# Optimization experiments

Hardware: AMD Instinct MI355X
Metric: run time of the kernel (lower is better)

The kernel has to match this reference:

```python
import jax, jax.numpy as jnp
import numpy as np

WIDTH = 1024

def setup_inputs() -> dict:
    key = jax.random.key(0)
    ks = jax.random.split(key, 5)
    x = jax.random.normal(ks[0], (4, 4096, WIDTH), dtype=jnp.float32)
    # LayerNorm params
    ln_gamma = jnp.ones((WIDTH,), dtype=jnp.float32)
    ln_beta = jnp.zeros((WIDTH,), dtype=jnp.float32)
    # Linear params (torch nn.Linear init: U(-1/sqrt(fan_in), 1/sqrt(fan_in)))
    bound = 1.0 / np.sqrt(WIDTH)
    w1 = jax.random.uniform(ks[1], (WIDTH, WIDTH), jnp.float32, -bound, bound)
    b1 = jax.random.uniform(ks[2], (WIDTH,), jnp.float32, -bound, bound)
    w2 = jax.random.uniform(ks[3], (WIDTH, WIDTH), jnp.float32, -bound, bound)
    b2 = jax.random.uniform(ks[4], (WIDTH,), jnp.float32, -bound, bound)
    return {"x": x, "ln_gamma": ln_gamma, "ln_beta": ln_beta,
            "w1": w1, "b1": b1, "w2": w2, "b2": b2}

def _layernorm(x, gamma, beta, eps=1e-5):
    mu = jnp.mean(x, axis=-1, keepdims=True)
    var = jnp.mean(jnp.square(x - mu), axis=-1, keepdims=True)
    return (x - mu) * jax.lax.rsqrt(var + eps) * gamma + beta

def reference(x, ln_gamma, ln_beta, w1, b1, w2, b2):
    # Pre-norm residual MLP: x + W2 @ gelu(W1 @ LN(x) + b1) + b2
    h = _layernorm(x, ln_gamma, ln_beta)
    h = jnp.einsum('bsd,ed->bse', h, w1) + b1  # w stored as [out, in] like torch
    h = jax.nn.gelu(h, approximate=False)      # torch nn.GELU default = exact erf
    # dropout p=0.0 -> identity
    h = jnp.einsum('bsd,ed->bse', h, w2) + b2
    return x + h
```

## Files before the change

kernel.cpp:

```cpp
#include <hip/hip_runtime.h>
#include <hip/hip_bf16.h>
#include <math.h>

typedef __bf16 bf16x8 __attribute__((ext_vector_type(8)));
typedef float f32x4 __attribute__((ext_vector_type(4)));

#define GAS __attribute__((address_space(1)))
#define LAS __attribute__((address_space(3)))

static __device__ __forceinline__ void load16(const void* g, void* l) {
    __builtin_amdgcn_global_load_lds((const GAS void*)g, (LAS void*)l, 16, 0, 0);
}

struct __align__(8) bh4 { __hip_bfloat16 x, y, z, w; };

__global__ __launch_bounds__(256) void pre_kernel(
        const float* __restrict__ x, const float* __restrict__ gamma,
        const float* __restrict__ beta, const float* __restrict__ w1,
        const float* __restrict__ w2, __hip_bfloat16* __restrict__ hn,
        __hip_bfloat16* __restrict__ w1b, __hip_bfloat16* __restrict__ w2b, int nln) {
    if ((int)blockIdx.x >= nln) {
        const int i = (blockIdx.x - nln) * 256 + threadIdx.x;
        float4 a = ((const float4*)w1)[i];
        float4 b = ((const float4*)w2)[i];
        bh4 r1, r2;
        r1.x = __float2bfloat16(a.x); r1.y = __float2bfloat16(a.y);
        r1.z = __float2bfloat16(a.z); r1.w = __float2bfloat16(a.w);
        r2.x = __float2bfloat16(b.x); r2.y = __float2bfloat16(b.y);
        r2.z = __float2bfloat16(b.z); r2.w = __float2bfloat16(b.w);
        ((bh4*)w1b)[i] = r1;
        ((bh4*)w2b)[i] = r2;
        return;
    }
    const int row  = (blockIdx.x << 2) + (threadIdx.x >> 6);
    const int lane = threadIdx.x & 63;
    const float4* px = (const float4*)(x + (size_t)row * 1024);
    float4 v[4];
    float s = 0.f;
#pragma unroll
    for (int i = 0; i < 4; ++i) {
        v[i] = px[lane + (i << 6)];
        s += v[i].x + v[i].y + v[i].z + v[i].w;
    }
#pragma unroll
    for (int o = 32; o; o >>= 1) s += __shfl_xor(s, o, 64);
    const float mu = s * (1.0f / 1024.0f);
    float vs = 0.f;
#pragma unroll
    for (int i = 0; i < 4; ++i) {
        float a = v[i].x - mu, b = v[i].y - mu, c = v[i].z - mu, d = v[i].w - mu;
        vs += a * a + b * b + c * c + d * d;
    }
#pragma unroll
    for (int o = 32; o; o >>= 1) vs += __shfl_xor(vs, o, 64);
    const float rs = rsqrtf(vs * (1.0f / 1024.0f) + 1e-5f);
    const float4* pg = (const float4*)gamma;
    const float4* pb = (const float4*)beta;
    bh4* po = (bh4*)(hn + (size_t)row * 1024);
#pragma unroll
    for (int i = 0; i < 4; ++i) {
        const int idx = lane + (i << 6);
        float4 g = pg[idx], bb = pb[idx];
        bh4 r;
        r.x = __float2bfloat16((v[i].x - mu) * rs * g.x + bb.x);
        r.y = __float2bfloat16((v[i].y - mu) * rs * g.y + bb.y);
        r.z = __float2bfloat16((v[i].z - mu) * rs * g.z + bb.z);
        r.w = __float2bfloat16((v[i].w - mu) * rs * g.w + bb.w);
        po[idx] = r;
    }
}

template <int EPI>
__global__ __launch_bounds__(256) void gemm_kernel(
        const __hip_bfloat16* __restrict__ A,
        const __hip_bfloat16* __restrict__ B,
        const float* __restrict__ bias,
        const float* __restrict__ resid,
        __hip_bfloat16* __restrict__ outb,
        float* __restrict__ outf) {
    constexpr int K = 1024, N = 1024;
    __shared__ __align__(16) char sA[16384];
    __shared__ __align__(16) char sB[16384];

    const int tid  = threadIdx.x;
    const int lane = tid & 63;
    const int w    = tid >> 6;
    const int wm   = (w >> 1) * 64;
    const int wn   = (w & 1) * 64;
    const int bm   = blockIdx.x * 128;
    const int bn   = blockIdx.y * 128;

    const int f = lane & 15;
    const int h = lane >> 4;

    const int srow = tid >> 3;
    const int lA_chunk = (tid & 7) ^ (srow & 7);
    const int lB_chunk = (tid & 7) ^ ((tid >> 5) & 7);
    const __hip_bfloat16* sa = A + (size_t)(bm + srow) * K + lA_chunk * 8;
    const __hip_bfloat16* sb = B + (size_t)(bn + srow) * K + lB_chunk * 8;
    char* dA = sA + tid * 16;
    char* dB = sB + tid * 16;

    const int pxk = (f & 7) * 16;
    const int px0 = (h * 16) ^ pxk;
    const int px1 = ((4 + h) * 16) ^ pxk;
    const char* aBase = sA + (wm + f) * 128;
    const char* bBase = sB + (wn + 4 * f) * 128;

    f32x4 acc[4][4] = {};

    for (int kt = 0; kt < K; kt += 64) {
#pragma unroll
        for (int q = 0; q < 4; ++q) {
            load16(sa + kt + q * 32 * K, dA + q * 4096);
            load16(sb + kt + q * 32 * K, dB + q * 4096);
        }
        __syncthreads();
#pragma unroll
        for (int c = 0; c < 2; ++c) {
            const int px = c ? px1 : px0;
            bf16x8 af[4], bf[4];
#pragma unroll
            for (int i = 0; i < 4; ++i)
                af[i] = *(const bf16x8*)(aBase + i * 2048 + px);
#pragma unroll
            for (int j = 0; j < 4; ++j)
                bf[j] = *(const bf16x8*)(bBase + j * 128 + px);
#pragma unroll
            for (int i = 0; i < 4; ++i)
#pragma unroll
                for (int j = 0; j < 4; ++j)
                    acc[i][j] = __builtin_amdgcn_mfma_f32_16x16x32_bf16(af[i], bf[j], acc[i][j], 0, 0, 0);
        }
        __syncthreads();
    }

    const int colb = bn + wn + f * 4;
    const float4 bias4 = *(const float4*)(bias + colb);
#pragma unroll
    for (int i = 0; i < 4; ++i) {
#pragma unroll
        for (int r = 0; r < 4; ++r) {
            const size_t grow = (size_t)(bm + wm + i * 16 + h * 4 + r);
            float v0 = acc[i][0][r] + bias4.x;
            float v1 = acc[i][1][r] + bias4.y;
            float v2 = acc[i][2][r] + bias4.z;
            float v3 = acc[i][3][r] + bias4.w;
            if (EPI == 0) {
                bh4 o;
                o.x = __float2bfloat16(0.5f * v0 * (1.0f + erff(v0 * 0.70710678118654752f)));
                o.y = __float2bfloat16(0.5f * v1 * (1.0f + erff(v1 * 0.70710678118654752f)));
                o.z = __float2bfloat16(0.5f * v2 * (1.0f + erff(v2 * 0.70710678118654752f)));
                o.w = __float2bfloat16(0.5f * v3 * (1.0f + erff(v3 * 0.70710678118654752f)));
                *(bh4*)(outb + grow * N + colb) = o;
            } else {
                const float4 rs = *(const float4*)(resid + grow * N + colb);
                float4 o = {v0 + rs.x, v1 + rs.y, v2 + rs.z, v3 + rs.w};
                *(float4*)(outf + grow * N + colb) = o;
            }
        }
    }
}

extern "C" void kernel_launch(void* const* d_in, const int* in_sizes, int n_in,
                              void* d_out, int out_size, void* d_ws, size_t ws_size,
                              hipStream_t stream) {
    const float* x     = (const float*)d_in[0];
    const float* gamma = (const float*)d_in[1];
    const float* beta  = (const float*)d_in[2];
    const float* w1    = (const float*)d_in[3];
    const float* b1    = (const float*)d_in[4];
    const float* w2    = (const float*)d_in[5];
    const float* b2    = (const float*)d_in[6];
    float* out = (float*)d_out;

    const int M = in_sizes[0] / 1024;

    char* ws = (char*)d_ws;
    __hip_bfloat16* hn  = (__hip_bfloat16*)ws;
    __hip_bfloat16* h1  = (__hip_bfloat16*)(ws + (size_t)M * 2048);
    __hip_bfloat16* w1b = (__hip_bfloat16*)(ws + (size_t)M * 4096);
    __hip_bfloat16* w2b = (__hip_bfloat16*)(ws + (size_t)M * 4096 + 2097152);

    const int nln = M / 4;
    pre_kernel<<<nln + 1024, 256, 0, stream>>>(x, gamma, beta, w1, w2, hn, w1b, w2b, nln);
    gemm_kernel<0><<<dim3(M / 128, 8), 256, 0, stream>>>(hn, w1b, b1, nullptr, h1, nullptr);
    gemm_kernel<1><<<dim3(M / 128, 8), 256, 0, stream>>>(h1, w2b, b2, x, nullptr, out);
}
```

Measured before the change: 227.3 us.

## Replace GEMM with 256x256 tile, 8-wave, double-buffered LDS pipelined kernel

Replaces the 128x128 single-buffered GEMM with a 256x256 tile kernel using 512 threads, 128 KB of LDS split into two buffers, and a hand-scheduled ping-pong pipeline. Global-to-LDS loads for the next k-tile are interleaved with MFMA phases using explicit barriers, waitcnts, sched_barriers and setprio. The aim is to overlap memory traffic with matrix math and raise data reuse per tile. The cost is fewer blocks (64x4 grid) and fragile manual synchronisation, and the 128 KB of LDS per block could limit occupancy.

```diff
diff --git a/kernel.cpp b/kernel.cpp
--- a/kernel.cpp
+++ b/kernel.cpp
@@ -70,8 +70,66 @@
     }
 }
 
+#define SCB() __builtin_amdgcn_sched_barrier(0)
+#define PHASE_MID() do { __builtin_amdgcn_s_barrier(); SCB(); \
+    asm volatile("s_waitcnt lgkmcnt(0)" ::: "memory"); SCB(); } while (0)
+#define PHASE_END() do { __builtin_amdgcn_s_barrier(); SCB(); } while (0)
+#define VMW(n) do { asm volatile("s_waitcnt vmcnt(" #n ")" ::: "memory"); SCB(); } while (0)
+
+__device__ __forceinline__ void rdA(const char* base, bf16x8 (&aF)[4][2], int px0, int px1) {
+#pragma unroll
+    for (int ii = 0; ii < 4; ++ii) {
+        aF[ii][0] = *(const bf16x8*)(base + ii * 2048 + px0);
+        aF[ii][1] = *(const bf16x8*)(base + ii * 2048 + px1);
+    }
+}
+__device__ __forceinline__ void rdB(const char* base, bf16x8 (&bF)[2][2], int px0, int px1) {
+#pragma unroll
+    for (int jj = 0; jj < 2; ++jj) {
+        bF[jj][0] = *(const bf16x8*)(base + jj * 128 + px0);
+        bF[jj][1] = *(const bf16x8*)(base + jj * 128 + px1);
+    }
+}
+template <int MI, int NI>
+__device__ __forceinline__ void mfmaQ(f32x4 (&acc)[8][4], const bf16x8 (&aF)[4][2],
+                                      const bf16x8 (&bF)[2][2]) {
+    __builtin_amdgcn_s_setprio(1);
+#pragma unroll
+    for (int ii = 0; ii < 4; ++ii)
+#pragma unroll
+        for (int jj = 0; jj < 2; ++jj) {
+            acc[MI * 4 + ii][NI * 2 + jj] = __builtin_amdgcn_mfma_f32_16x16x32_bf16(
+                aF[ii][0], bF[jj][0], acc[MI * 4 + ii][NI * 2 + jj], 0, 0, 0);
+            acc[MI * 4 + ii][NI * 2 + jj] = __builtin_amdgcn_mfma_f32_16x16x32_bf16(
+                aF[ii][1], bF[jj][1], acc[MI * 4 + ii][NI * 2 + jj], 0, 0, 0);
+        }
+    __builtin_amdgcn_s_setprio(0);
+}
+
+#define TILE(CUR, OTH, KOFF, SA_EN, SB_EN) do { \
+    const char* aB_ = aRd + (CUR) * 32768; \
+    const char* bB_ = bRd + (CUR) * 32768; \
+    rdA(aB_, aF, px0, px1); \
+    rdB(bB_, bF0, px0, px1); \
+    if (SA_EN) { load16(aS0 + (KOFF) + 64, dA + (OTH) * 32768); \
+                 load16(aS1 + (KOFF) + 64, dA + (OTH) * 32768 + 8192); } \
+    PHASE_MID(); mfmaQ<0, 0>(acc, aF, bF0); PHASE_END(); \
+    rdB(bB_ + 256, bF1, px0, px1); \
+    if (SA_EN) { load16(aS0 + 131072 + (KOFF) + 64, dA + (OTH) * 32768 + 16384); \
+                 load16(aS1 + 131072 + (KOFF) + 64, dA + (OTH) * 32768 + 24576); } \
+    PHASE_MID(); mfmaQ<0, 1>(acc, aF, bF1); PHASE_END(); \
+    rdA(aB_ + 8192, aF, px0, px1); \
+    if (SB_EN) { load16(bS0 + (KOFF) + 128, dB + (CUR) * 32768); \
+                 load16(bS1 + (KOFF) + 128, dB + (CUR) * 32768 + 8192); } \
+    PHASE_MID(); mfmaQ<1, 1>(acc, aF, bF1); PHASE_END(); \
+    if (SB_EN) { load16(bS0 + 131072 + (KOFF) + 128, dB + (CUR) * 32768 + 16384); \
+                 load16(bS1 + 131072 + (KOFF) + 128, dB + (CUR) * 32768 + 24576); } \
+    __builtin_amdgcn_s_barrier(); SCB(); \
+    mfmaQ<1, 0>(acc, aF, bF0); \
+} while (0)
+
 template <int EPI>
-__global__ __launch_bounds__(256) void gemm_kernel(
+__global__ __launch_bounds__(512, 2) void gemm256(
         const __hip_bfloat16* __restrict__ A,
         const __hip_bfloat16* __restrict__ B,
         const float* __restrict__ bias,
@@ -79,69 +137,65 @@
         __hip_bfloat16* __restrict__ outb,
         float* __restrict__ outf) {
     constexpr int K = 1024, N = 1024;
-    __shared__ __align__(16) char sA[16384];
-    __shared__ __align__(16) char sB[16384];
+    __shared__ __align__(16) char lds[131072];
+    char* sA = lds;
+    char* sB = lds + 65536;
 
     const int tid  = threadIdx.x;
     const int lane = tid & 63;
     const int w    = tid >> 6;
-    const int wm   = (w >> 1) * 64;
-    const int wn   = (w & 1) * 64;
-    const int bm   = blockIdx.x * 128;
-    const int bn   = blockIdx.y * 128;
-
-    const int f = lane & 15;
-    const int h = lane >> 4;
-
-    const int srow = tid >> 3;
-    const int lA_chunk = (tid & 7) ^ (srow & 7);
-    const int lB_chunk = (tid & 7) ^ ((tid >> 5) & 7);
-    const __hip_bfloat16* sa = A + (size_t)(bm + srow) * K + lA_chunk * 8;
-    const __hip_bfloat16* sb = B + (size_t)(bn + srow) * K + lB_chunk * 8;
+    const int wr   = w >> 2;
+    const int wc   = w & 3;
+    const int f    = lane & 15;
+    const int h    = lane >> 4;
+    const int bm   = blockIdx.x * 256;
+    const int bn   = blockIdx.y * 256;
+
+    const int cid0 = tid, cid1 = tid + 512;
+    const __hip_bfloat16* aS0 = A + (size_t)(bm + (cid0 >> 3)) * K + (((cid0 & 7) ^ ((cid0 >> 3) & 7)) << 3);
+    const __hip_bfloat16* aS1 = A + (size_t)(bm + (cid1 >> 3)) * K + (((cid1 & 7) ^ ((cid1 >> 3) & 7)) << 3);
+    const __hip_bfloat16* bS0 = B + (size_t)(bn + (cid0 >> 3)) * K + (((cid0 & 7) ^ ((cid0 >> 5) & 7)) << 3);
+    const __hip_bfloat16* bS1 = B + (size_t)(bn + (cid1 >> 3)) * K + (((cid1 & 7) ^ ((cid1 >> 5) & 7)) << 3);
     char* dA = sA + tid * 16;
     char* dB = sB + tid * 16;
 
     const int pxk = (f & 7) * 16;
     const int px0 = (h * 16) ^ pxk;
     const int px1 = ((4 + h) * 16) ^ pxk;
-    const char* aBase = sA + (wm + f) * 128;
-    const char* bBase = sB + (wn + 4 * f) * 128;
-
-    f32x4 acc[4][4] = {};
-
-    for (int kt = 0; kt < K; kt += 64) {
-#pragma unroll
-        for (int q = 0; q < 4; ++q) {
-            load16(sa + kt + q * 32 * K, dA + q * 4096);
-            load16(sb + kt + q * 32 * K, dB + q * 4096);
-        }
-        __syncthreads();
-#pragma unroll
-        for (int c = 0; c < 2; ++c) {
-            const int px = c ? px1 : px0;
-            bf16x8 af[4], bf[4];
-#pragma unroll
-            for (int i = 0; i < 4; ++i)
-                af[i] = *(const bf16x8*)(aBase + i * 2048 + px);
-#pragma unroll
-            for (int j = 0; j < 4; ++j)
-                bf[j] = *(const bf16x8*)(bBase + j * 128 + px);
-#pragma unroll
-            for (int i = 0; i < 4; ++i)
-#pragma unroll
-                for (int j = 0; j < 4; ++j)
-                    acc[i][j] = __builtin_amdgcn_mfma_f32_16x16x32_bf16(af[i], bf[j], acc[i][j], 0, 0, 0);
-        }
-        __syncthreads();
-    }
-
-    const int colb = bn + wn + f * 4;
+    const char* aRd = sA + (size_t)(wr * 128 + f) * 128;
+    const char* bRd = sB + (size_t)(wc * 64 + 4 * f) * 128;
+
+    f32x4 acc[8][4] = {};
+    bf16x8 aF[4][2], bF0[2][2], bF1[2][2];
+
+    load16(bS0, dB);                  load16(bS1, dB + 8192);
+    load16(bS0 + 131072, dB + 16384); load16(bS1 + 131072, dB + 24576);
+    load16(aS0, dA);                  load16(aS1, dA + 8192);
+    load16(aS0 + 131072, dA + 16384); load16(aS1 + 131072, dA + 24576);
+    load16(bS0 + 64, dB + 32768);             load16(bS1 + 64, dB + 32768 + 8192);
+    load16(bS0 + 131072 + 64, dB + 32768 + 16384); load16(bS1 + 131072 + 64, dB + 32768 + 24576);
+    VMW(4);
+    PHASE_END();
+
+#pragma unroll 1
+    for (int it = 0; it < 7; ++it) {
+        const int k0 = it << 7;
+        TILE(0, 1, k0, true, true);
+        VMW(4); PHASE_END();
+        TILE(1, 0, k0 + 64, true, true);
+        VMW(4); PHASE_END();
+    }
+    TILE(0, 1, 896, true, false);
+    VMW(0); PHASE_END();
+    TILE(1, 0, 960, false, false);
+
+    const int colb = bn + wc * 64 + f * 4;
     const float4 bias4 = *(const float4*)(bias + colb);
 #pragma unroll
-    for (int i = 0; i < 4; ++i) {
+    for (int i = 0; i < 8; ++i) {
 #pragma unroll
         for (int r = 0; r < 4; ++r) {
-            const size_t grow = (size_t)(bm + wm + i * 16 + h * 4 + r);
+            const size_t grow = (size_t)(bm + wr * 128 + i * 16 + h * 4 + r);
             float v0 = acc[i][0][r] + bias4.x;
             float v1 = acc[i][1][r] + bias4.y;
             float v2 = acc[i][2][r] + bias4.z;
@@ -184,6 +238,6 @@
 
     const int nln = M / 4;
     pre_kernel<<<nln + 1024, 256, 0, stream>>>(x, gamma, beta, w1, w2, hn, w1b, w2b, nln);
-    gemm_kernel<0><<<dim3(M / 128, 8), 256, 0, stream>>>(hn, w1b, b1, nullptr, h1, nullptr);
-    gemm_kernel<1><<<dim3(M / 128, 8), 256, 0, stream>>>(h1, w2b, b2, x, nullptr, out);
-}
+    gemm256<0><<<dim3(M / 256, 4), 512, 0, stream>>>(hn, w1b, b1, nullptr, h1, nullptr);
+    gemm256<1><<<dim3(M / 256, 4), 512, 0, stream>>>(h1, w2b, b2, x, nullptr, out);
+}
```

Measured after the change: 216.2 us. 1.05x faster.

## Double-buffer GEMM LDS tiles with explicit waitcnt scheduling and fast GELU

Applied to the files above, without the earlier changes.

The GEMM kernel now uses two LDS buffers so global-to-LDS loads for the next K-tile are issued while MFMAs consume the current tile. Explicit waitcnt, sched barriers and setprio control the interleaving, and launch bounds request two blocks per CU. The erff-based GELU is replaced with an Abramowitz-Stegun polynomial erf using a hardware reciprocal and fast exp, which lowers epilogue cost but adds a small approximation error. The doubled LDS footprint (64KB per block) may limit occupancy.

```diff
diff --git a/kernel.cpp b/kernel.cpp
--- a/kernel.cpp
+++ b/kernel.cpp
@@ -70,8 +70,62 @@
     }
 }
 
+__device__ __forceinline__ float gelu_exact(float v) {
+    const float ax = fabsf(v) * 0.70710678118654752f;
+    const float t  = __builtin_amdgcn_rcpf(__builtin_fmaf(0.3275911f, ax, 1.0f));
+    float p = __builtin_fmaf(1.061405429f, t, -1.453152027f);
+    p = __builtin_fmaf(p, t, 1.421413741f);
+    p = __builtin_fmaf(p, t, -0.284496736f);
+    p = __builtin_fmaf(p, t, 0.254829592f);
+    p *= t;
+    const float e  = __expf(-ax * ax);
+    const float er = __builtin_fmaf(-p, e, 1.0f);
+    return 0.5f * v * (1.0f + copysignf(er, v));
+}
+
+#define SCB() __builtin_amdgcn_sched_barrier(0)
+#define BAR() do { __builtin_amdgcn_s_barrier(); SCB(); } while (0)
+#define LGKM(n) do { asm volatile("s_waitcnt lgkmcnt(" #n ")" ::: "memory"); SCB(); } while (0)
+#define VMW(n) do { asm volatile("s_waitcnt vmcnt(" #n ")" ::: "memory"); SCB(); } while (0)
+
+__device__ __forceinline__ void rd4(const char* base, int stride, bf16x8 (&v)[4]) {
+#pragma unroll
+    for (int i = 0; i < 4; ++i) v[i] = *(const bf16x8*)(base + i * stride);
+}
+
+#define MFMA16(AF, BF) do { __builtin_amdgcn_s_setprio(1); \
+    _Pragma("unroll") for (int i2 = 0; i2 < 4; ++i2) \
+    _Pragma("unroll") for (int j2 = 0; j2 < 4; ++j2) \
+        acc[i2][j2] = __builtin_amdgcn_mfma_f32_16x16x32_bf16(AF[i2], BF[j2], acc[i2][j2], 0, 0, 0); \
+    __builtin_amdgcn_s_setprio(0); } while (0)
+
+#define TILE128(CUR, OTH, KOFF, S1) do { \
+    const char* aB_ = aBase + (CUR) * 16384; \
+    const char* bB_ = bBase + (CUR) * 16384; \
+    rd4(aB_ + px0, 2048, af0); SCB(); \
+    rd4(bB_ + px0, 128, bf0); SCB(); \
+    rd4(aB_ + px1, 2048, af1); SCB(); \
+    rd4(bB_ + px1, 128, bf1); SCB(); \
+    if (S1) { \
+        char* dAo = dA + (OTH) * 16384; \
+        char* dBo = dB + (OTH) * 16384; \
+        load16(sa + (KOFF) + 64,             dAo); \
+        load16(sb + (KOFF) + 64,             dBo); \
+        load16(sa + (KOFF) + 64 + 32 * 1024, dAo + 4096); \
+        load16(sb + (KOFF) + 64 + 32 * 1024, dBo + 4096); \
+        load16(sa + (KOFF) + 64 + 64 * 1024, dAo + 8192); \
+        load16(sb + (KOFF) + 64 + 64 * 1024, dBo + 8192); \
+        load16(sa + (KOFF) + 64 + 96 * 1024, dAo + 12288); \
+        load16(sb + (KOFF) + 64 + 96 * 1024, dBo + 12288); \
+    } \
+    LGKM(8); \
+    MFMA16(af0, bf0); \
+    LGKM(0); \
+    MFMA16(af1, bf1); \
+} while (0)
+
 template <int EPI>
-__global__ __launch_bounds__(256) void gemm_kernel(
+__global__ __launch_bounds__(256, 2) void gemm128(
         const __hip_bfloat16* __restrict__ A,
         const __hip_bfloat16* __restrict__ B,
         const float* __restrict__ bias,
@@ -79,8 +133,8 @@
         __hip_bfloat16* __restrict__ outb,
         float* __restrict__ outf) {
     constexpr int K = 1024, N = 1024;
-    __shared__ __align__(16) char sA[16384];
-    __shared__ __align__(16) char sB[16384];
+    __shared__ __align__(16) char sA[32768];
+    __shared__ __align__(16) char sB[32768];
 
     const int tid  = threadIdx.x;
     const int lane = tid & 63;
@@ -108,32 +162,26 @@
     const char* bBase = sB + (wn + 4 * f) * 128;
 
     f32x4 acc[4][4] = {};
-
-    for (int kt = 0; kt < K; kt += 64) {
-#pragma unroll
-        for (int q = 0; q < 4; ++q) {
-            load16(sa + kt + q * 32 * K, dA + q * 4096);
-            load16(sb + kt + q * 32 * K, dB + q * 4096);
-        }
-        __syncthreads();
-#pragma unroll
-        for (int c = 0; c < 2; ++c) {
-            const int px = c ? px1 : px0;
-            bf16x8 af[4], bf[4];
-#pragma unroll
-            for (int i = 0; i < 4; ++i)
-                af[i] = *(const bf16x8*)(aBase + i * 2048 + px);
-#pragma unroll
-            for (int j = 0; j < 4; ++j)
-                bf[j] = *(const bf16x8*)(bBase + j * 128 + px);
-#pragma unroll
-            for (int i = 0; i < 4; ++i)
-#pragma unroll
-                for (int j = 0; j < 4; ++j)
-                    acc[i][j] = __builtin_amdgcn_mfma_f32_16x16x32_bf16(af[i], bf[j], acc[i][j], 0, 0, 0);
-        }
-        __syncthreads();
-    }
+    bf16x8 af0[4], af1[4], bf0[4], bf1[4];
+
+    load16(sa, dA);                 load16(sb, dB);
+    load16(sa + 32 * 1024, dA + 4096); load16(sb + 32 * 1024, dB + 4096);
+    load16(sa + 64 * 1024, dA + 8192); load16(sb + 64 * 1024, dB + 8192);
+    load16(sa + 96 * 1024, dA + 12288); load16(sb + 96 * 1024, dB + 12288);
+    VMW(0);
+    BAR();
+
+#pragma unroll 1
+    for (int it = 0; it < 7; ++it) {
+        const int k0 = it << 7;
+        TILE128(0, 1, k0, true);
+        VMW(0); BAR();
+        TILE128(1, 0, k0 + 64, true);
+        VMW(0); BAR();
+    }
+    TILE128(0, 1, 896, true);
+    VMW(0); BAR();
+    TILE128(1, 0, 960, false);
 
     const int colb = bn + wn + f * 4;
     const float4 bias4 = *(const float4*)(bias + colb);
@@ -148,10 +196,10 @@
             float v3 = acc[i][3][r] + bias4.w;
             if (EPI == 0) {
                 bh4 o;
-                o.x = __float2bfloat16(0.5f * v0 * (1.0f + erff(v0 * 0.70710678118654752f)));
-                o.y = __float2bfloat16(0.5f * v1 * (1.0f + erff(v1 * 0.70710678118654752f)));
-                o.z = __float2bfloat16(0.5f * v2 * (1.0f + erff(v2 * 0.70710678118654752f)));
-                o.w = __float2bfloat16(0.5f * v3 * (1.0f + erff(v3 * 0.70710678118654752f)));
+                o.x = __float2bfloat16(gelu_exact(v0));
+                o.y = __float2bfloat16(gelu_exact(v1));
+                o.z = __float2bfloat16(gelu_exact(v2));
+                o.w = __float2bfloat16(gelu_exact(v3));
                 *(bh4*)(outb + grow * N + colb) = o;
             } else {
                 const float4 rs = *(const float4*)(resid + grow * N + colb);
@@ -184,6 +232,6 @@
 
     const int nln = M / 4;
     pre_kernel<<<nln + 1024, 256, 0, stream>>>(x, gamma, beta, w1, w2, hn, w1b, w2b, nln);
-    gemm_kernel<0><<<dim3(M / 128, 8), 256, 0, stream>>>(hn, w1b, b1, nullptr, h1, nullptr);
-    gemm_kernel<1><<<dim3(M / 128, 8), 256, 0, stream>>>(h1, w2b, b2, x, nullptr, out);
-}
+    gemm128<0><<<dim3(M / 128, 8), 256, 0, stream>>>(hn, w1b, b1, nullptr, h1, nullptr);
+    gemm128<1><<<dim3(M / 128, 8), 256, 0, stream>>>(h1, w2b, b2, x, nullptr, out);
+}
```

Result: faster. 209.4 us (-7.9%).
